# Kernel tuning notes

Hardware: AMD Instinct MI355X
Metric: run time of the kernel (lower is better)

## Reference

```python
import jax, jax.numpy as jnp
import numpy as np

N, IN, OUT, T = 65536, 256, 256, 8


def setup_inputs() -> dict:
    key = jax.random.key(0)
    k1, k2, k3, k4 = jax.random.split(key, 4)
    x = jax.random.normal(k1, (N, IN), dtype=jnp.float32)
    types = jax.random.randint(k2, (N,), 0, T, dtype=jnp.int32)
    # xavier_uniform for W: limit = sqrt(6 / (fan_in + fan_out)) with fan computed
    # on the last two dims (out_size, in_size)
    limit = float(np.sqrt(6.0 / (IN + OUT)))
    W = jax.random.uniform(k3, (T, OUT, IN), dtype=jnp.float32, minval=-limit, maxval=limit)
    # original inits b to zeros; use small random values so the bias path is exercised
    b = 0.01 * jax.random.normal(k4, (T, OUT), dtype=jnp.float32)
    return {"x": x, "types": types, "W": W, "b": b}


def reference(x, types, W, b):
    # out[i] = W[types[i]] @ x[i] + b[types[i]]
    # Grouped-GEMM expressed as a loop over the small fixed set of types,
    # avoiding the huge [N, OUT, IN] gather of W[types].
    num_types = W.shape[0]
    out = b[types]  # [N, OUT]
    for t in range(num_types):
        mask = (types == t)[:, None]  # [N, 1]
        out = out + jnp.where(mask, x @ W[t].T, jnp.float32(0.0))
    return out
```

## Files before the change

kernel.cpp:

```cpp
#include <hip/hip_runtime.h>
#include <hip/hip_bf16.h>
#include <stdint.h>


#define NROWS 65536
#define NTYPES 8
#define KDIM 256
#define ODIM 256
#define BM 128
#define BN 128
#define BK 64

typedef __attribute__((ext_vector_type(8))) short short8;
typedef __attribute__((ext_vector_type(4))) float f32x4;

__device__ __forceinline__ unsigned short f2bf(float f) {
    unsigned int u = __float_as_uint(f);
    u += 0x7fffu + ((u >> 16) & 1u);
    return (unsigned short)(u >> 16);
}

__global__ void prep_kernel(const float* __restrict__ W,
                            unsigned short* __restrict__ Wb,
                            int* __restrict__ cnt) {
    if (blockIdx.x == 0 && threadIdx.x < NTYPES) cnt[threadIdx.x] = 0;
    int i = blockIdx.x * 256 + threadIdx.x;
    float4 v = ((const float4*)W)[i];
    ushort4 p;
    p.x = f2bf(v.x); p.y = f2bf(v.y); p.z = f2bf(v.z); p.w = f2bf(v.w);
    ((ushort4*)Wb)[i] = p;
}

__global__ void bucket_kernel(const int* __restrict__ types,
                              int* __restrict__ cnt,
                              int* __restrict__ idx) {
    __shared__ int h[NTYPES];
    __shared__ int base[NTYPES];
    int i = blockIdx.x * 256 + threadIdx.x;
    if (threadIdx.x < NTYPES) h[threadIdx.x] = 0;
    __syncthreads();
    int t = types[i];
    int r = atomicAdd(&h[t], 1);
    __syncthreads();
    if (threadIdx.x < NTYPES)
        base[threadIdx.x] = atomicAdd(&cnt[threadIdx.x], h[threadIdx.x]);
    __syncthreads();
    idx[t * NROWS + base[t] + r] = i;
}

__global__ __launch_bounds__(256, 2)
void gemm_kernel(const float* __restrict__ x,
                 const float* __restrict__ bias,
                 const unsigned short* __restrict__ Wb,
                 const int* __restrict__ cnt,
                 const int* __restrict__ idx,
                 float* __restrict__ out) {
    const int t = blockIdx.z;
    const int count = cnt[t];
    const int m0 = blockIdx.x * BM;
    if (m0 >= count) return;
    const int n0 = blockIdx.y * BN;

    __shared__ int idx_s[BM];
    __shared__ float bias_s[BN];
    __shared__ unsigned short As[BM * BK];
    __shared__ unsigned short Bs[BN * BK];

    const int tid = threadIdx.x;

    if (tid < BM) {
        int m = m0 + tid;
        idx_s[tid] = (m < count) ? idx[t * NROWS + m] : 0;
    } else {
        bias_s[tid - BM] = bias[t * ODIM + n0 + (tid - BM)];
    }
    __syncthreads();

    const int wave = tid >> 6;
    const int lane = tid & 63;
    const int lr = lane & 15;
    const int lq = lane >> 4;
    const int wm = (wave >> 1) * 64;
    const int wn = (wave & 1) * 64;

    f32x4 acc[4][4] = {};

    const int srow = tid >> 4;
    const int sc   = tid & 15;

    char* AsB = (char*)As;
    char* BsB = (char*)Bs;

    for (int k0 = 0; k0 < KDIM; k0 += BK) {
        #pragma unroll
        for (int j = 0; j < 8; ++j) {
            int row = j * 16 + srow;
            const float4 v = *(const float4*)(x + (size_t)idx_s[row] * KDIM + k0 + sc * 4);
            ushort4 p;
            p.x = f2bf(v.x); p.y = f2bf(v.y); p.z = f2bf(v.z); p.w = f2bf(v.w);
            int ch = (sc >> 1) ^ (row & 7);
            *(ushort4*)(AsB + row * 128 + ch * 16 + (sc & 1) * 8) = p;
        }
        #pragma unroll
        for (int it = 0; it < 4; ++it) {
            int dbyte = wave * 4096 + it * 1024;
            int drow  = (dbyte >> 7) + (lane >> 3);
            int schunk = (lane & 7) ^ (lane >> 3);
            const unsigned short* src =
                Wb + (size_t)(t * ODIM + n0 + drow) * KDIM + k0 + schunk * 8;
            __builtin_amdgcn_global_load_lds(
                (const __attribute__((address_space(1))) void*)src,
                (__attribute__((address_space(3))) void*)(BsB + dbyte),
                16, 0, 0);
        }
        __syncthreads();

        #pragma unroll
        for (int kh = 0; kh < 2; ++kh) {
            short8 af[4], bf[4];
            #pragma unroll
            for (int i = 0; i < 4; ++i) {
                int arow = wm + i * 16 + lr;
                int ach = ((kh << 2) + lq) ^ (arow & 7);
                af[i] = *(const short8*)(AsB + arow * 128 + ach * 16);
            }
            #pragma unroll
            for (int i = 0; i < 4; ++i) {
                int brow = wn + i * 16 + lr;
                int bch = ((kh << 2) + lq) ^ (brow & 7);
                bf[i] = *(const short8*)(BsB + brow * 128 + bch * 16);
            }
            #pragma unroll
            for (int i = 0; i < 4; ++i)
                #pragma unroll
                for (int j = 0; j < 4; ++j)
                    acc[i][j] = __builtin_amdgcn_mfma_f32_16x16x32_bf16(
                        af[i], bf[j], acc[i][j], 0, 0, 0);
        }
        __syncthreads();
    }

    #pragma unroll
    for (int i = 0; i < 4; ++i) {
        int lmBase = wm + i * 16 + lq * 4;
        #pragma unroll
        for (int r = 0; r < 4; ++r) {
            int lm = lmBase + r;
            if (m0 + lm < count) {
                size_t orow = (size_t)idx_s[lm] * ODIM;
                #pragma unroll
                for (int j = 0; j < 4; ++j) {
                    int col = wn + j * 16 + lr;
                    out[orow + n0 + col] = acc[i][j][r] + bias_s[col];
                }
            }
        }
    }
}

extern "C" void kernel_launch(void* const* d_in, const int* in_sizes, int n_in,
                              void* d_out, int out_size, void* d_ws, size_t ws_size,
                              hipStream_t stream) {
    const float* x     = (const float*)d_in[0];
    const int*   types = (const int*)d_in[1];
    const float* W     = (const float*)d_in[2];
    const float* b     = (const float*)d_in[3];
    float* out = (float*)d_out;

    char* ws = (char*)d_ws;
    int* cnt = (int*)ws;
    int* idx = (int*)(ws + 1024);
    unsigned short* Wb = (unsigned short*)(ws + 1024 + (size_t)NTYPES * NROWS * sizeof(int));

    prep_kernel<<<512, 256, 0, stream>>>(W, Wb, cnt);
    bucket_kernel<<<NROWS / 256, 256, 0, stream>>>(types, cnt, idx);
    dim3 grid(NROWS / BM, ODIM / BN, NTYPES);
    gemm_kernel<<<grid, 256, 0, stream>>>(x, b, Wb, cnt, idx, out);
}
```

Baseline: 142.9 us.

## Merge prep and bucket kernels, compact grouped GEMM grid, batch x loads

Combines the weight conversion and row bucketing into a single launch, using a memset to zero the counters. The GEMM grid changes from a padded per-type 3D grid, where most blocks exited early, to a compact 1D tile list that each block maps to a type by scanning the counts. x loads are issued after the weight async loads and are all gathered into registers before conversion, to overlap memory latency. The occupancy hint is raised to 4 blocks per CU, which may cause register spills.

```diff
diff --git a/kernel.cpp b/kernel.cpp
--- a/kernel.cpp
+++ b/kernel.cpp
@@ -1,5 +1,4 @@
 #include <hip/hip_runtime.h>
-#include <hip/hip_bf16.h>
 #include <stdint.h>
 
 
@@ -10,6 +9,7 @@
 #define BM 128
 #define BN 128
 #define BK 64
+#define MAX_TILES (NROWS / BM + NTYPES - 1)
 
 typedef __attribute__((ext_vector_type(8))) short short8;
 typedef __attribute__((ext_vector_type(4))) float f32x4;
@@ -20,45 +20,51 @@
     return (unsigned short)(u >> 16);
 }
 
-__global__ void prep_kernel(const float* __restrict__ W,
-                            unsigned short* __restrict__ Wb,
-                            int* __restrict__ cnt) {
-    if (blockIdx.x == 0 && threadIdx.x < NTYPES) cnt[threadIdx.x] = 0;
-    int i = blockIdx.x * 256 + threadIdx.x;
-    float4 v = ((const float4*)W)[i];
-    ushort4 p;
-    p.x = f2bf(v.x); p.y = f2bf(v.y); p.z = f2bf(v.z); p.w = f2bf(v.w);
-    ((ushort4*)Wb)[i] = p;
+__global__ void prep_bucket_kernel(const float* __restrict__ W,
+                                   unsigned short* __restrict__ Wb,
+                                   const int* __restrict__ types,
+                                   int* __restrict__ cnt,
+                                   int* __restrict__ idx) {
+    const int b = blockIdx.x;
+    if (b < 512) {
+        int i = b * 256 + threadIdx.x;
+        float4 v = ((const float4*)W)[i];
+        ushort4 p;
+        p.x = f2bf(v.x); p.y = f2bf(v.y); p.z = f2bf(v.z); p.w = f2bf(v.w);
+        ((ushort4*)Wb)[i] = p;
+    } else {
+        __shared__ int h[NTYPES];
+        __shared__ int base[NTYPES];
+        int i = (b - 512) * 256 + threadIdx.x;
+        if (threadIdx.x < NTYPES) h[threadIdx.x] = 0;
+        __syncthreads();
+        int t = types[i];
+        int r = atomicAdd(&h[t], 1);
+        __syncthreads();
+        if (threadIdx.x < NTYPES)
+            base[threadIdx.x] = atomicAdd(&cnt[threadIdx.x], h[threadIdx.x]);
+        __syncthreads();
+        idx[t * NROWS + base[t] + r] = i;
+    }
 }
 
-__global__ void bucket_kernel(const int* __restrict__ types,
-                              int* __restrict__ cnt,
-                              int* __restrict__ idx) {
-    __shared__ int h[NTYPES];
-    __shared__ int base[NTYPES];
-    int i = blockIdx.x * 256 + threadIdx.x;
-    if (threadIdx.x < NTYPES) h[threadIdx.x] = 0;
-    __syncthreads();
-    int t = types[i];
-    int r = atomicAdd(&h[t], 1);
-    __syncthreads();
-    if (threadIdx.x < NTYPES)
-        base[threadIdx.x] = atomicAdd(&cnt[threadIdx.x], h[threadIdx.x]);
-    __syncthreads();
-    idx[t * NROWS + base[t] + r] = i;
-}
-
-__global__ __launch_bounds__(256, 2)
+__global__ __launch_bounds__(256, 4)
 void gemm_kernel(const float* __restrict__ x,
                  const float* __restrict__ bias,
                  const unsigned short* __restrict__ Wb,
                  const int* __restrict__ cnt,
                  const int* __restrict__ idx,
                  float* __restrict__ out) {
-    const int t = blockIdx.z;
-    const int count = cnt[t];
-    const int m0 = blockIdx.x * BM;
-    if (m0 >= count) return;
+    const int bid = blockIdx.x;
+    int t = -1, m0 = 0, count = 0, accum = 0;
+    #pragma unroll
+    for (int i = 0; i < NTYPES; ++i) {
+        int c = cnt[i];
+        int ntile = (c + BM - 1) / BM;
+        if (t < 0 && bid < accum + ntile) { t = i; m0 = (bid - accum) * BM; count = c; }
+        accum += ntile;
+    }
+    if (t < 0) return;
     const int n0 = blockIdx.y * BN;
 
     __shared__ int idx_s[BM];
@@ -93,15 +99,6 @@
 
     for (int k0 = 0; k0 < KDIM; k0 += BK) {
         #pragma unroll
-        for (int j = 0; j < 8; ++j) {
-            int row = j * 16 + srow;
-            const float4 v = *(const float4*)(x + (size_t)idx_s[row] * KDIM + k0 + sc * 4);
-            ushort4 p;
-            p.x = f2bf(v.x); p.y = f2bf(v.y); p.z = f2bf(v.z); p.w = f2bf(v.w);
-            int ch = (sc >> 1) ^ (row & 7);
-            *(ushort4*)(AsB + row * 128 + ch * 16 + (sc & 1) * 8) = p;
-        }
-        #pragma unroll
         for (int it = 0; it < 4; ++it) {
             int dbyte = wave * 4096 + it * 1024;
             int drow  = (dbyte >> 7) + (lane >> 3);
@@ -112,6 +109,21 @@
                 (const __attribute__((address_space(1))) void*)src,
                 (__attribute__((address_space(3))) void*)(BsB + dbyte),
                 16, 0, 0);
+        }
+        float4 av[8];
+        #pragma unroll
+        for (int j = 0; j < 8; ++j) {
+            int row = j * 16 + srow;
+            av[j] = *(const float4*)(x + (size_t)idx_s[row] * KDIM + k0 + sc * 4);
+        }
+        #pragma unroll
+        for (int j = 0; j < 8; ++j) {
+            int row = j * 16 + srow;
+            ushort4 p;
+            p.x = f2bf(av[j].x); p.y = f2bf(av[j].y);
+            p.z = f2bf(av[j].z); p.w = f2bf(av[j].w);
+            int ch = (sc >> 1) ^ (row & 7);
+            *(ushort4*)(AsB + row * 128 + ch * 16 + (sc & 1) * 8) = p;
         }
         __syncthreads();
 
@@ -172,8 +184,8 @@
     int* idx = (int*)(ws + 1024);
     unsigned short* Wb = (unsigned short*)(ws + 1024 + (size_t)NTYPES * NROWS * sizeof(int));
 
-    prep_kernel<<<512, 256, 0, stream>>>(W, Wb, cnt);
-    bucket_kernel<<<NROWS / 256, 256, 0, stream>>>(types, cnt, idx);
-    dim3 grid(NROWS / BM, ODIM / BN, NTYPES);
+    hipMemsetAsync(cnt, 0, NTYPES * sizeof(int), stream);
+    prep_bucket_kernel<<<768, 256, 0, stream>>>(W, Wb, types, cnt, idx);
+    dim3 grid(MAX_TILES, ODIM / BN);
     gemm_kernel<<<grid, 256, 0, stream>>>(x, b, Wb, cnt, idx, out);
 }
```

Result: faster. 137.5 us (-3.7%).
